# Kernel tuning notes

Hardware: AMD Instinct MI355X
Metric: run time of the kernel (lower is better)

The kernel has to match this reference:

```python
import jax, jax.numpy as jnp
import numpy as np

B, C, HD, H, W = 4, 64, 64, 64, 64  # batch, input_dim, hidden_dim, spatial


def conv1x1(x, w, b):
    # x: [B, Cin, H, W], w: [Cout, Cin], b: [Cout]
    return jnp.einsum('oc,bchw->bohw', w, x) + b[None, :, None, None]


def setup_inputs() -> dict:
    key = jax.random.key(0)
    ks = jax.random.split(key, 16)
    sc = lambda cin: 1.0 / np.sqrt(cin)
    d = {
        'h': jax.random.normal(ks[0], (B, C, H, W), jnp.float32),
        'm': jax.random.normal(ks[1], (B, C, H, W), jnp.float32),
        'Wq': jax.random.normal(ks[2], (HD, C), jnp.float32) * sc(C),
        'bq': jnp.zeros((HD,), jnp.float32),
        'Wk': jax.random.normal(ks[3], (HD, C), jnp.float32) * sc(C),
        'bk': jnp.zeros((HD,), jnp.float32),
        'Wk2': jax.random.normal(ks[4], (HD, C), jnp.float32) * sc(C),
        'bk2': jnp.zeros((HD,), jnp.float32),
        'Wv': jax.random.normal(ks[5], (C, C), jnp.float32) * sc(C),
        'bv': jnp.zeros((C,), jnp.float32),
        'Wv2': jax.random.normal(ks[6], (C, C), jnp.float32) * sc(C),
        'bv2': jnp.zeros((C,), jnp.float32),
        'Wz': jax.random.normal(ks[7], (2 * C, 2 * C), jnp.float32) * sc(2 * C),
        'bz': jnp.zeros((2 * C,), jnp.float32),
        'Wm': jax.random.normal(ks[8], (3 * C, 3 * C), jnp.float32) * sc(3 * C),
        'bm': jnp.zeros((3 * C,), jnp.float32),
    }
    return d


def reference(h, m, Wq, bq, Wk, bk, Wk2, bk2, Wv, bv, Wv2, bv2, Wz, bz, Wm, bm):
    b, c, hh, ww = h.shape
    n = hh * ww
    K_h = conv1x1(h, Wk, bk).reshape(b, HD, n)            # [B, HD, N]
    Q_h = conv1x1(h, Wq, bq).reshape(b, HD, n).transpose(0, 2, 1)  # [B, N, HD]
    V_h = conv1x1(h, Wv, bv).reshape(b, c, n)             # [B, C, N]
    K_m = conv1x1(m, Wk2, bk2).reshape(b, HD, n)
    V_m = conv1x1(m, Wv2, bv2).reshape(b, c, n)

    A_h = jax.nn.softmax(jnp.einsum('bnd,bdk->bnk', Q_h, K_h), axis=-1)  # [B, N, N]
    Z_h = jnp.einsum('bnk,bck->bcn', A_h, V_h).reshape(b, c, hh, ww)
    A_m = jax.nn.softmax(jnp.einsum('bnd,bdk->bnk', Q_h, K_m), axis=-1)
    Z_m = jnp.einsum('bnk,bck->bcn', A_m, V_m).reshape(b, c, hh, ww)

    Z = conv1x1(jnp.concatenate([Z_h, Z_m], axis=1), Wz, bz)   # [B, 2C, H, W]
    combined = conv1x1(jnp.concatenate([Z, h], axis=1), Wm, bm)  # [B, 3C, H, W]
    mo, mg, mi = jnp.split(combined, 3, axis=1)
    mi = jax.nn.sigmoid(mi)
    new_m = (1.0 - mi) * m + mi * jnp.tanh(mg)
    new_h = jax.nn.sigmoid(mo) * new_m
    return (new_h, new_m)
```

## Files before the change

kernel.cpp:

```cpp
#include <hip/hip_runtime.h>

#define BN 4
#define NN 4096
#define SPLITK 4
#define KTILE 64
#define LOG2E 1.44269504f
#define MFIX 36.0f

typedef __attribute__((ext_vector_type(8))) __bf16 bf16x8;
typedef __attribute__((ext_vector_type(8))) short s16x8;
typedef __attribute__((ext_vector_type(4))) float f32x4;
typedef unsigned short u16;

__device__ __forceinline__ u16 f2bf(float x) {
  unsigned int u = __builtin_bit_cast(unsigned int, x);
  u = (u + 0x7fffu + ((u >> 16) & 1u)) >> 16;
  return (u16)u;
}
__device__ __forceinline__ u16 f2bfs(float x) {
  __bf16 b = (__bf16)x;
  return __builtin_bit_cast(u16, b);
}
__device__ __forceinline__ float bf2f(u16 s) {
  unsigned int u = ((unsigned int)s) << 16;
  return __builtin_bit_cast(float, u);
}

__device__ __forceinline__ float fexp2(float x) {
#if defined(__HIP_DEVICE_COMPILE__) && __has_builtin(__builtin_amdgcn_exp2f)
  return __builtin_amdgcn_exp2f(x);
#else
  return __builtin_exp2f(x);
#endif
}

__device__ __forceinline__ f32x4 mfma32(bf16x8 a, bf16x8 b, f32x4 c) {
#if defined(__HIP_DEVICE_COMPILE__)
  return __builtin_amdgcn_mfma_f32_16x16x32_bf16(a, b, c, 0, 0, 0);
#else
  (void)a; (void)b;
  return c;
#endif
}

__device__ __forceinline__ void gld16(const u16* g, u16* l) {
#if defined(__HIP_DEVICE_COMPILE__)
  __builtin_amdgcn_global_load_lds(
      (const __attribute__((address_space(1))) void*)g,
      (__attribute__((address_space(3))) void*)l, 16, 0, 0);
#else
  (void)g; (void)l;
#endif
}

#if defined(__HIP_DEVICE_COMPILE__)
#define SETPRIO(p) __builtin_amdgcn_s_setprio(p)
#else
#define SETPRIO(p)
#endif

__global__ __launch_bounds__(256) void fuse_w2_kernel(
    const float* __restrict__ Wz, const float* __restrict__ bz,
    const float* __restrict__ Wm, const float* __restrict__ bm,
    const float* __restrict__ Wq, const float* __restrict__ Wk,
    const float* __restrict__ Wk2, const float* __restrict__ Wv,
    const float* __restrict__ Wv2,
    u16* __restrict__ Wbig, float* __restrict__ bbig, u16* __restrict__ Wall) {
  __shared__ float wrow[128];
  __shared__ float bzs[128];
  int t = threadIdx.x;
  if (blockIdx.x >= 192) {
    int pid = blockIdx.x - 192;
    const float* Wsrc = pid == 0 ? Wq : pid == 1 ? Wk : pid == 2 ? Wk2 : pid == 3 ? Wv : Wv2;
    float sc = (pid == 0) ? LOG2E : 1.f;
#pragma unroll
    for (int i = 0; i < 16; ++i) {
      int idx = t * 16 + i;
      float w = Wsrc[idx] * sc;
      u16 hu = f2bf(w);
      Wall[pid * 4096 + idx] = hu;
      Wall[5 * 4096 + pid * 4096 + idx] = f2bf(w - bf2f(hu));
    }
    return;
  }
  int o = blockIdx.x;
  if (t < 128) { wrow[t] = Wm[o * 192 + t]; bzs[t] = bz[t]; }
  __syncthreads();
  if (t < 128) {
    float s = 0.f;
#pragma unroll 4
    for (int j = 0; j < 128; ++j) s = fmaf(wrow[j], Wz[j * 128 + t], s);
    Wbig[o * 192 + t] = f2bf(s);
  } else if (t < 192) {
    Wbig[o * 192 + t] = f2bf(Wm[o * 192 + t]);
  } else if (t == 192) {
    float s = bm[o];
    for (int j = 0; j < 128; ++j) s = fmaf(wrow[j], bzs[j], s);
    bbig[o] = s;
  }
}

__global__ __launch_bounds__(256) void proj7_kernel(
    const u16* __restrict__ Wall,
    const float* __restrict__ bq, const float* __restrict__ bk,
    const float* __restrict__ bk2, const float* __restrict__ bv,
    const float* __restrict__ bv2,
    const float* __restrict__ h, const float* __restrict__ m,
    u16* __restrict__ Q, u16* __restrict__ Kh, u16* __restrict__ Km,
    u16* __restrict__ Vh, u16* __restrict__ Vm, u16* __restrict__ hT) {
  __shared__ float xs[64][65];
  int blk = blockIdx.x;
  int nt = blk & 63, b = (blk >> 6) & 3, src_m = blk >> 8;
  const float* src = src_m ? m : h;
  int t = threadIdx.x, lane = t & 63, w = t >> 6, col = lane & 15, quad = lane >> 4;
  int n0 = nt * 64;
  {
    int c0 = w * 16, nl = lane;
#pragma unroll
    for (int i = 0; i < 16; ++i)
      xs[c0 + i][nl] = src[((size_t)(b * 64) + c0 + i) * NN + n0 + nl];
  }
  __syncthreads();
  int nloc = w * 16 + col;
  bf16x8 xh[2], xl[2];
#pragma unroll
  for (int half = 0; half < 2; ++half) {
    bf16x8 hh, ll;
#pragma unroll
    for (int j = 0; j < 8; ++j) {
      float x = xs[half * 32 + quad * 8 + j][nloc];
      u16 hu = f2bf(x);
      hh[j] = __builtin_bit_cast(__bf16, hu);
      ll[j] = (__bf16)(x - bf2f(hu));
    }
    xh[half] = hh; xl[half] = ll;
  }
  if (!src_m) {
    int cj = lane & 7, nr = lane >> 3;
#pragma unroll
    for (int it = 0; it < 2; ++it) {
      int n = w * 16 + it * 8 + nr;
      bf16x8 hi8;
#pragma unroll
      for (int i = 0; i < 8; ++i)
        hi8[i] = __builtin_bit_cast(__bf16, f2bf(xs[cj * 8 + i][n]));
      *(bf16x8*)(void*)(hT + ((size_t)b * NN + n0 + n) * 64 + cj * 8) = hi8;
    }
  }
  int glob_n = n0 + nloc;
  auto do_proj = [&](int pid, const float* bias, u16* dstQK, u16* dstV) {
    const u16* Whi = Wall + pid * 4096;
    const u16* Wlo = Wall + 5 * 4096 + pid * 4096;
    float sc = (pid == 0) ? LOG2E : 1.f;
#pragma unroll
    for (int ot = 0; ot < 4; ++ot) {
      size_t wb = (size_t)(ot * 16 + col) * 64 + quad * 8;
      bf16x8 wh0 = *(const bf16x8*)(const void*)(Whi + wb);
      bf16x8 wh1 = *(const bf16x8*)(const void*)(Whi + wb + 32);
      bf16x8 wl0 = *(const bf16x8*)(const void*)(Wlo + wb);
      bf16x8 wl1 = *(const bf16x8*)(const void*)(Wlo + wb + 32);
      float4 b4 = *(const float4*)(bias + ot * 16 + quad * 4);
      f32x4 c = {b4.x * sc, b4.y * sc, b4.z * sc, b4.w * sc};
      c = mfma32(wh0, xh[0], c);
      c = mfma32(wh1, xh[1], c);
      c = mfma32(wh0, xl[0], c);
      c = mfma32(wh1, xl[1], c);
      c = mfma32(wl0, xh[0], c);
      c = mfma32(wl1, xh[1], c);
      if (dstQK) {
        uint2 p;
        p.x = (unsigned)f2bf(c[0]) | ((unsigned)f2bf(c[1]) << 16);
        p.y = (unsigned)f2bf(c[2]) | ((unsigned)f2bf(c[3]) << 16);
        *(uint2*)(void*)(dstQK + ((size_t)b * NN + glob_n) * 64 + ot * 16 + quad * 4) = p;
      } else {
        size_t base = ((size_t)b << 18) + (size_t)(glob_n >> 5) * 2048 + ot * 512 +
                      (size_t)((glob_n >> 3) & 3) * 128 + (glob_n & 7);
#pragma unroll
        for (int r = 0; r < 4; ++r) dstV[base + (quad * 4 + r) * 8] = f2bf(c[r]);
      }
    }
  };
  if (!src_m) {
    do_proj(0, bq, Q, nullptr);
    do_proj(1, bk, Kh, nullptr);
    do_proj(3, bv, nullptr, Vh);
  } else {
    do_proj(2, bk2, Km, nullptr);
    do_proj(4, bv2, nullptr, Vm);
  }
}

__global__ __launch_bounds__(256, 4) void flash11_kernel(
    const u16* __restrict__ Qg, const u16* __restrict__ Khg,
    const u16* __restrict__ Kmg, const u16* __restrict__ Vhg,
    const u16* __restrict__ Vmg, u16* __restrict__ Opart,
    float* __restrict__ Lpart) {
  __shared__ u16 Kl[2][4096];
  __shared__ u16 Vl[2][4096];
  int blk = blockIdx.x;
  int combo = blk & 31, qt = blk >> 5;
  int attn = combo & 1, b = (combo >> 1) & 3, split = combo >> 3;
  const u16* K = (attn ? Kmg : Khg) + (size_t)b * NN * 64;
  const u16* V = (attn ? Vmg : Vhg) + ((size_t)b << 18);
  int t = threadIdx.x, wave = t >> 6, lane = t & 63, col = lane & 15, quad = lane >> 4;
  int row0 = qt * 128 + wave * 32;

  bf16x8 bq[2][2];
#pragma unroll
  for (int g = 0; g < 2; ++g) {
    const u16* qp = Qg + (size_t)b * NN * 64 + (size_t)(row0 + g * 16 + col) * 64 + quad * 8;
    bq[g][0] = *(const bf16x8*)(const void*)qp;
    bq[g][1] = *(const bf16x8*)(const void*)(qp + 32);
  }

  f32x4 O[2][4];
#pragma unroll
  for (int g = 0; g < 2; ++g)
#pragma unroll
    for (int i = 0; i < 4; ++i) O[g][i] = f32x4{0.f, 0.f, 0.f, 0.f};
  f32x4 Lacc[2];
  Lacc[0] = f32x4{0.f, 0.f, 0.f, 0.f};
  Lacc[1] = f32x4{0.f, 0.f, 0.f, 0.f};
  const f32x4 minit = {-MFIX, -MFIX, -MFIX, -MFIX};
  s16x8 onesv;
#pragma unroll
  for (int i = 0; i < 8; ++i) onesv[i] = (short)0x3F80;
  bf16x8 ones8 = __builtin_bit_cast(bf16x8, onesv);
  int sp = split * 8 + b * 2 + attn;

  const int kbase = split * (NN / SPLITK);
  const int TILES = NN / SPLITK / KTILE;

#define STAGE(BUF, K0)                                                           \
  _Pragma("unroll") for (int jj = 0; jj < 2; ++jj) {                             \
    int p = jj * 256 + t;                                                        \
    int krow_ = p >> 3;                                                          \
    int kj_ = (p & 7) ^ (krow_ & 7);                                             \
    int s5_ = krow_ & 31;                                                        \
    int tr_ = (krow_ & 32) | ((s5_ & 12) << 1) | (((s5_ >> 4) & 1) << 2) | (s5_ & 3); \
    gld16(K + (size_t)((K0) + tr_) * 64 + kj_ * 8, &Kl[BUF][p * 8]);             \
    gld16(V + (size_t)(K0) * 64 + p * 8, &Vl[BUF][p * 8]);                       \
  }

  STAGE(0, kbase);

  for (int kt = 0; kt < TILES; ++kt) {
    __syncthreads();
    int cur = kt & 1;
    if (kt + 1 < TILES) { STAGE(cur ^ 1, kbase + (kt + 1) * KTILE); }
    const u16* Kb = &Kl[cur][0];
    const u16* Vb = &Vl[cur][0];
    f32x4 St[4][2];
    SETPRIO(1);
#pragma unroll
    for (int nt = 0; nt < 4; ++nt) {
      int row = nt * 16 + col;
      int ph0 = row * 8 + (quad ^ (col & 7));
      int ph1 = row * 8 + ((4 + quad) ^ (col & 7));
      bf16x8 a0 = *(const bf16x8*)(const void*)(Kb + ph0 * 8);
      bf16x8 a1 = *(const bf16x8*)(const void*)(Kb + ph1 * 8);
#pragma unroll
      for (int g = 0; g < 2; ++g) {
        f32x4 acc = mfma32(a0, bq[g][0], minit);
        acc = mfma32(a1, bq[g][1], acc);
        St[nt][g] = acc;
      }
    }
    SETPRIO(0);
    bf16x8 pa[2][2];
#pragma unroll
    for (int grp = 0; grp < 2; ++grp)
#pragma unroll
      for (int g = 0; g < 2; ++g) {
        s16x8 pf;
#pragma unroll
        for (int r = 0; r < 4; ++r) {
          pf[r] = (short)f2bfs(fexp2(St[2 * grp][g][r]));
          pf[r + 4] = (short)f2bfs(fexp2(St[2 * grp + 1][g][r]));
        }
        bf16x8 p8 = __builtin_bit_cast(bf16x8, pf);
        pa[grp][g] = p8;
        Lacc[g] = mfma32(p8, ones8, Lacc[g]);
      }
    const u16* vbase = Vb + lane * 8;
    SETPRIO(1);
#pragma unroll
    for (int grp = 0; grp < 2; ++grp)
#pragma unroll
      for (int ct = 0; ct < 4; ++ct) {
        bf16x8 vf = *(const bf16x8*)(const void*)(vbase + grp * 2048 + ct * 512);
        O[0][ct] = mfma32(pa[grp][0], vf, O[0][ct]);
        O[1][ct] = mfma32(pa[grp][1], vf, O[1][ct]);
      }
    SETPRIO(0);
  }
#undef STAGE

#pragma unroll
  for (int g = 0; g < 2; ++g) {
#pragma unroll
    for (int ct = 0; ct < 4; ++ct)
#pragma unroll
      for (int r = 0; r < 4; ++r) {
        size_t q = (size_t)row0 + g * 16 + quad * 4 + r;
        Opart[((size_t)sp * NN + q) * 64 + ct * 16 + col] = f2bfs(O[g][ct][r]);
      }
    if (col == 0) {
#pragma unroll
      for (int r = 0; r < 4; ++r)
        Lpart[(size_t)sp * NN + row0 + g * 16 + quad * 4 + r] = Lacc[g][r];
    }
  }
}

__global__ __launch_bounds__(256) void epi3_kernel(
    const u16* __restrict__ Wb, const float* __restrict__ bb,
    const u16* __restrict__ Opart, const float* __restrict__ Lpart,
    const u16* __restrict__ hT, const float* __restrict__ mglob,
    float* __restrict__ out) {
  int blk = blockIdx.x;
  int ng = blk * 16;
  int b = ng >> 12;
  int t = threadIdx.x, wave = t >> 6, lane = t & 63, col = lane & 15, quad = lane >> 4;
  int qb = (ng & (NN - 1)) + col;
  float Lh = 0.f, Lm = 0.f;
#pragma unroll
  for (int s = 0; s < SPLITK; ++s) {
    Lh += Lpart[(size_t)(s * 8 + b * 2) * NN + qb];
    Lm += Lpart[(size_t)(s * 8 + b * 2 + 1) * NN + qb];
  }
  float invLh = 1.f / Lh;
  float invLm = 1.f / Lm;
  size_t nrow = ((size_t)ng + col) * 64;
  bf16x8 bfr[6];
#define MERGEF(DST, ATTN, OFF, INVL)                                             \
  {                                                                              \
    float s8_[8] = {0.f, 0.f, 0.f, 0.f, 0.f, 0.f, 0.f, 0.f};                     \
    _Pragma("unroll") for (int sp_ = 0; sp_ < SPLITK; ++sp_) {                   \
      const u16* p_ =                                                            \
          Opart + ((size_t)(sp_ * 8 + b * 2 + (ATTN)) * NN + qb) * 64 + (OFF);   \
      bf16x8 a_ = *(const bf16x8*)(const void*)p_;                               \
      _Pragma("unroll") for (int i = 0; i < 8; ++i) s8_[i] += (float)a_[i];      \
    }                                                                            \
    bf16x8 r_;                                                                   \
    _Pragma("unroll") for (int i = 0; i < 8; ++i)                                \
      r_[i] = (__bf16)(s8_[i] * (INVL));                                         \
    DST = r_;                                                                    \
  }
  MERGEF(bfr[0], 0, quad * 8, invLh);
  MERGEF(bfr[1], 0, 32 + quad * 8, invLh);
  MERGEF(bfr[2], 1, quad * 8, invLm);
  MERGEF(bfr[3], 1, 32 + quad * 8, invLm);
#undef MERGEF
  bfr[4] = *(const bf16x8*)(const void*)(hT + nrow + quad * 8);
  bfr[5] = *(const bf16x8*)(const void*)(hT + nrow + 32 + quad * 8);
  f32x4 acc[3];
#pragma unroll
  for (int j = 0; j < 3; ++j) {
    int mt = wave + j * 4;
#pragma unroll
    for (int r = 0; r < 4; ++r) acc[j][r] = bb[mt * 16 + quad * 4 + r];
  }
#pragma unroll
  for (int ks = 0; ks < 6; ++ks) {
#pragma unroll
    for (int j = 0; j < 3; ++j) {
      int mt = wave + j * 4;
      bf16x8 af = *(const bf16x8*)(const void*)(Wb + (size_t)(mt * 16 + col) * 192 + ks * 32 + quad * 8);
      acc[j] = mfma32(af, bfr[ks], acc[j]);
    }
  }
  int nloc = (ng & (NN - 1)) + col;
#pragma unroll
  for (int r = 0; r < 4; ++r) {
    int o = wave * 16 + quad * 4 + r;
    float mo = acc[0][r], mgt = acc[1][r], mi = acc[2][r];
    float si = 1.f / (1.f + fexp2(-mi * LOG2E));
    float tg = 1.f - 2.f / (fexp2(2.f * LOG2E * mgt) + 1.f);
    float mv = mglob[(size_t)(b * 64 + o) * NN + nloc];
    float nm = (1.f - si) * mv + si * tg;
    float nh = nm / (1.f + fexp2(-mo * LOG2E));
    out[(size_t)(b * 64 + o) * NN + nloc] = nh;
    out[(size_t)BN * 64 * NN + (size_t)(b * 64 + o) * NN + nloc] = nm;
  }
}

extern "C" void kernel_launch(void* const* d_in, const int* in_sizes, int n_in,
                              void* d_out, int out_size, void* d_ws, size_t ws_size,
                              hipStream_t stream) {
  const float* h = (const float*)d_in[0];
  const float* m = (const float*)d_in[1];
  const float* Wq = (const float*)d_in[2];
  const float* bq = (const float*)d_in[3];
  const float* Wk = (const float*)d_in[4];
  const float* bk = (const float*)d_in[5];
  const float* Wk2 = (const float*)d_in[6];
  const float* bk2 = (const float*)d_in[7];
  const float* Wv = (const float*)d_in[8];
  const float* bv = (const float*)d_in[9];
  const float* Wv2 = (const float*)d_in[10];
  const float* bv2 = (const float*)d_in[11];
  const float* Wz = (const float*)d_in[12];
  const float* bz = (const float*)d_in[13];
  const float* Wm = (const float*)d_in[14];
  const float* bm = (const float*)d_in[15];
  float* out = (float*)d_out;

  size_t off = 0;
  auto alloc = [&](size_t bytes) {
    void* p = (char*)d_ws + off;
    off += (bytes + 255) & ~(size_t)255;
    return p;
  };
  const size_t bn64 = (size_t)BN * NN * 64;
  u16* Q  = (u16*)alloc(bn64 * 2);
  u16* Kh = (u16*)alloc(bn64 * 2);
  u16* Km = (u16*)alloc(bn64 * 2);
  u16* Vh = (u16*)alloc(bn64 * 2);
  u16* Vm = (u16*)alloc(bn64 * 2);
  u16* hT = (u16*)alloc(bn64 * 2);
  u16* Opart = (u16*)alloc((size_t)SPLITK * 8 * NN * 64 * 2);
  float* Lpart = (float*)alloc((size_t)SPLITK * 8 * NN * 4);
  u16* Wbigbf = (u16*)alloc(192 * 192 * 2);
  float* bbig = (float*)alloc(192 * 4);
  u16* Wall = (u16*)alloc((size_t)2 * 5 * 4096 * 2);
  (void)ws_size; (void)in_sizes; (void)n_in; (void)out_size;

  fuse_w2_kernel<<<197, 256, 0, stream>>>(Wz, bz, Wm, bm, Wq, Wk, Wk2, Wv, Wv2,
                                          Wbigbf, bbig, Wall);
  proj7_kernel<<<2 * BN * 64, 256, 0, stream>>>(Wall, bq, bk, bk2, bv, bv2, h, m,
                                                Q, Kh, Km, Vh, Vm, hT);
  flash11_kernel<<<32 * 32, 256, 0, stream>>>(Q, Kh, Km, Vh, Vm, Opart, Lpart);
  epi3_kernel<<<(BN * NN) / 16, 256, 0, stream>>>(Wbigbf, bbig, Opart, Lpart, hT, m, out);
}
```

Measured before the change: 167.7 us.

## Use 2 waves per block with 64 query rows per wave in flash kernel

The flash attention kernel now launches 128 threads per block, and each of the 2 waves handles 64 query rows instead of 32, so each K/V fragment read from LDS feeds twice as many MFMAs. K fragments are loaded once per tile and reused across two query-group passes, and global-to-LDS staging is spread over fewer threads. This cuts LDS read traffic per FLOP but raises register pressure (O and bq double) and halves the waves per block, which may lower occupancy and latency hiding.

```diff
diff --git a/kernel.cpp b/kernel.cpp
--- a/kernel.cpp
+++ b/kernel.cpp
@@ -190,7 +190,7 @@
   }
 }
 
-__global__ __launch_bounds__(256, 4) void flash11_kernel(
+__global__ __launch_bounds__(128, 2) void flash12_kernel(
     const u16* __restrict__ Qg, const u16* __restrict__ Khg,
     const u16* __restrict__ Kmg, const u16* __restrict__ Vhg,
     const u16* __restrict__ Vmg, u16* __restrict__ Opart,
@@ -203,24 +203,24 @@
   const u16* K = (attn ? Kmg : Khg) + (size_t)b * NN * 64;
   const u16* V = (attn ? Vmg : Vhg) + ((size_t)b << 18);
   int t = threadIdx.x, wave = t >> 6, lane = t & 63, col = lane & 15, quad = lane >> 4;
-  int row0 = qt * 128 + wave * 32;
-
-  bf16x8 bq[2][2];
-#pragma unroll
-  for (int g = 0; g < 2; ++g) {
+  int row0 = qt * 128 + wave * 64;
+
+  bf16x8 bq[4][2];
+#pragma unroll
+  for (int g = 0; g < 4; ++g) {
     const u16* qp = Qg + (size_t)b * NN * 64 + (size_t)(row0 + g * 16 + col) * 64 + quad * 8;
     bq[g][0] = *(const bf16x8*)(const void*)qp;
     bq[g][1] = *(const bf16x8*)(const void*)(qp + 32);
   }
 
-  f32x4 O[2][4];
-#pragma unroll
-  for (int g = 0; g < 2; ++g)
+  f32x4 O[4][4];
+#pragma unroll
+  for (int g = 0; g < 4; ++g)
 #pragma unroll
     for (int i = 0; i < 4; ++i) O[g][i] = f32x4{0.f, 0.f, 0.f, 0.f};
-  f32x4 Lacc[2];
-  Lacc[0] = f32x4{0.f, 0.f, 0.f, 0.f};
-  Lacc[1] = f32x4{0.f, 0.f, 0.f, 0.f};
+  f32x4 Lacc[4];
+#pragma unroll
+  for (int g = 0; g < 4; ++g) Lacc[g] = f32x4{0.f, 0.f, 0.f, 0.f};
   const f32x4 minit = {-MFIX, -MFIX, -MFIX, -MFIX};
   s16x8 onesv;
 #pragma unroll
@@ -232,8 +232,8 @@
   const int TILES = NN / SPLITK / KTILE;
 
 #define STAGE(BUF, K0)                                                           \
-  _Pragma("unroll") for (int jj = 0; jj < 2; ++jj) {                             \
-    int p = jj * 256 + t;                                                        \
+  _Pragma("unroll") for (int jj = 0; jj < 4; ++jj) {                             \
+    int p = jj * 128 + t;                                                        \
     int krow_ = p >> 3;                                                          \
     int kj_ = (p & 7) ^ (krow_ & 7);                                             \
     int s5_ = krow_ & 31;                                                        \
@@ -250,38 +250,43 @@
     if (kt + 1 < TILES) { STAGE(cur ^ 1, kbase + (kt + 1) * KTILE); }
     const u16* Kb = &Kl[cur][0];
     const u16* Vb = &Vl[cur][0];
-    f32x4 St[4][2];
-    SETPRIO(1);
+    bf16x8 a0[4], a1[4];
 #pragma unroll
     for (int nt = 0; nt < 4; ++nt) {
       int row = nt * 16 + col;
-      int ph0 = row * 8 + (quad ^ (col & 7));
-      int ph1 = row * 8 + ((4 + quad) ^ (col & 7));
-      bf16x8 a0 = *(const bf16x8*)(const void*)(Kb + ph0 * 8);
-      bf16x8 a1 = *(const bf16x8*)(const void*)(Kb + ph1 * 8);
-#pragma unroll
-      for (int g = 0; g < 2; ++g) {
-        f32x4 acc = mfma32(a0, bq[g][0], minit);
-        acc = mfma32(a1, bq[g][1], acc);
-        St[nt][g] = acc;
-      }
-    }
-    SETPRIO(0);
-    bf16x8 pa[2][2];
-#pragma unroll
-    for (int grp = 0; grp < 2; ++grp)
-#pragma unroll
-      for (int g = 0; g < 2; ++g) {
-        s16x8 pf;
-#pragma unroll
-        for (int r = 0; r < 4; ++r) {
-          pf[r] = (short)f2bfs(fexp2(St[2 * grp][g][r]));
-          pf[r + 4] = (short)f2bfs(fexp2(St[2 * grp + 1][g][r]));
+      a0[nt] = *(const bf16x8*)(const void*)(Kb + (row * 8 + (quad ^ (col & 7))) * 8);
+      a1[nt] = *(const bf16x8*)(const void*)(Kb + (row * 8 + ((4 + quad) ^ (col & 7))) * 8);
+    }
+    bf16x8 pa[2][4];
+#pragma unroll
+    for (int gp = 0; gp < 2; ++gp) {
+      f32x4 St[4][2];
+      SETPRIO(1);
+#pragma unroll
+      for (int nt = 0; nt < 4; ++nt)
+#pragma unroll
+        for (int gg = 0; gg < 2; ++gg) {
+          int g = gp * 2 + gg;
+          f32x4 acc = mfma32(a0[nt], bq[g][0], minit);
+          acc = mfma32(a1[nt], bq[g][1], acc);
+          St[nt][gg] = acc;
         }
-        bf16x8 p8 = __builtin_bit_cast(bf16x8, pf);
-        pa[grp][g] = p8;
-        Lacc[g] = mfma32(p8, ones8, Lacc[g]);
-      }
+      SETPRIO(0);
+#pragma unroll
+      for (int grp = 0; grp < 2; ++grp)
+#pragma unroll
+        for (int gg = 0; gg < 2; ++gg) {
+          s16x8 pf;
+#pragma unroll
+          for (int r = 0; r < 4; ++r) {
+            pf[r] = (short)f2bfs(fexp2(St[2 * grp][gg][r]));
+            pf[r + 4] = (short)f2bfs(fexp2(St[2 * grp + 1][gg][r]));
+          }
+          bf16x8 p8 = __builtin_bit_cast(bf16x8, pf);
+          pa[grp][gp * 2 + gg] = p8;
+          Lacc[gp * 2 + gg] = mfma32(p8, ones8, Lacc[gp * 2 + gg]);
+        }
+    }
     const u16* vbase = Vb + lane * 8;
     SETPRIO(1);
 #pragma unroll
@@ -289,15 +294,15 @@
 #pragma unroll
       for (int ct = 0; ct < 4; ++ct) {
         bf16x8 vf = *(const bf16x8*)(const void*)(vbase + grp * 2048 + ct * 512);
-        O[0][ct] = mfma32(pa[grp][0], vf, O[0][ct]);
-        O[1][ct] = mfma32(pa[grp][1], vf, O[1][ct]);
+#pragma unroll
+        for (int g = 0; g < 4; ++g) O[g][ct] = mfma32(pa[grp][g], vf, O[g][ct]);
       }
     SETPRIO(0);
   }
 #undef STAGE
 
 #pragma unroll
-  for (int g = 0; g < 2; ++g) {
+  for (int g = 0; g < 4; ++g) {
 #pragma unroll
     for (int ct = 0; ct < 4; ++ct)
 #pragma unroll
@@ -430,6 +435,6 @@
                                           Wbigbf, bbig, Wall);
   proj7_kernel<<<2 * BN * 64, 256, 0, stream>>>(Wall, bq, bk, bk2, bv, bv2, h, m,
                                                 Q, Kh, Km, Vh, Vm, hT);
-  flash11_kernel<<<32 * 32, 256, 0, stream>>>(Q, Kh, Km, Vh, Vm, Opart, Lpart);
+  flash12_kernel<<<32 * 32, 128, 0, stream>>>(Q, Kh, Km, Vh, Vm, Opart, Lpart);
   epi3_kernel<<<(BN * NN) / 16, 256, 0, stream>>>(Wbigbf, bbig, Opart, Lpart, hT, m, out);
 }
```

After: 169.7 us. No clear change (+1.2%).

## Software-pipeline PV matmul one tile behind QK with triple-buffered V

Applied to the files above, without the earlier changes.

Restructures the flash attention loop so that each iteration's P·V MFMAs use the probabilities from the previous tile, placed between the QK^T MFMAs and the exp/bf16 conversion of the current tile. The goal is to let the exp and convert work overlap with matrix-core work instead of serialising QK, softmax and PV. V gets a third shared-memory buffer so the previous tile's V is still resident while the next tile is being staged. Shared memory per block rises from 32 KB to 40 KB, which could reduce occupancy, and more registers stay live across iterations.

```diff
diff --git a/kernel.cpp b/kernel.cpp
--- a/kernel.cpp
+++ b/kernel.cpp
@@ -190,13 +190,13 @@
   }
 }
 
-__global__ __launch_bounds__(256, 4) void flash11_kernel(
+__global__ __launch_bounds__(256, 4) void flash13_kernel(
     const u16* __restrict__ Qg, const u16* __restrict__ Khg,
     const u16* __restrict__ Kmg, const u16* __restrict__ Vhg,
     const u16* __restrict__ Vmg, u16* __restrict__ Opart,
     float* __restrict__ Lpart) {
   __shared__ u16 Kl[2][4096];
-  __shared__ u16 Vl[2][4096];
+  __shared__ u16 Vl[3][4096];
   int blk = blockIdx.x;
   int combo = blk & 31, qt = blk >> 5;
   int attn = combo & 1, b = (combo >> 1) & 3, split = combo >> 3;
@@ -221,6 +221,11 @@
   f32x4 Lacc[2];
   Lacc[0] = f32x4{0.f, 0.f, 0.f, 0.f};
   Lacc[1] = f32x4{0.f, 0.f, 0.f, 0.f};
+  bf16x8 pa[2][2];
+#pragma unroll
+  for (int grp = 0; grp < 2; ++grp)
+#pragma unroll
+    for (int g = 0; g < 2; ++g) pa[grp][g] = bf16x8{};
   const f32x4 minit = {-MFIX, -MFIX, -MFIX, -MFIX};
   s16x8 onesv;
 #pragma unroll
@@ -231,25 +236,29 @@
   const int kbase = split * (NN / SPLITK);
   const int TILES = NN / SPLITK / KTILE;
 
-#define STAGE(BUF, K0)                                                           \
+#define STAGE(KB, VB, K0)                                                        \
   _Pragma("unroll") for (int jj = 0; jj < 2; ++jj) {                             \
     int p = jj * 256 + t;                                                        \
     int krow_ = p >> 3;                                                          \
     int kj_ = (p & 7) ^ (krow_ & 7);                                             \
     int s5_ = krow_ & 31;                                                        \
     int tr_ = (krow_ & 32) | ((s5_ & 12) << 1) | (((s5_ >> 4) & 1) << 2) | (s5_ & 3); \
-    gld16(K + (size_t)((K0) + tr_) * 64 + kj_ * 8, &Kl[BUF][p * 8]);             \
-    gld16(V + (size_t)(K0) * 64 + p * 8, &Vl[BUF][p * 8]);                       \
-  }
-
-  STAGE(0, kbase);
+    gld16(K + (size_t)((K0) + tr_) * 64 + kj_ * 8, (KB) + p * 8);                \
+    gld16(V + (size_t)(K0) * 64 + p * 8, (VB) + p * 8);                          \
+  }
+
+  STAGE(&Kl[0][0], &Vl[0][0], kbase);
+  int vs_cur = 0;
 
   for (int kt = 0; kt < TILES; ++kt) {
+    int cur = kt & 1;
+    int vs_nxt = (vs_cur == 2) ? 0 : vs_cur + 1;
+    int vs_prv = (vs_cur == 0) ? 2 : vs_cur - 1;
     __syncthreads();
-    int cur = kt & 1;
-    if (kt + 1 < TILES) { STAGE(cur ^ 1, kbase + (kt + 1) * KTILE); }
+    if (kt + 1 < TILES) {
+      STAGE(&Kl[cur ^ 1][0], &Vl[vs_nxt][0], kbase + (kt + 1) * KTILE);
+    }
     const u16* Kb = &Kl[cur][0];
-    const u16* Vb = &Vl[cur][0];
     f32x4 St[4][2];
     SETPRIO(1);
 #pragma unroll
@@ -267,7 +276,19 @@
       }
     }
     SETPRIO(0);
-    bf16x8 pa[2][2];
+    if (kt > 0) {
+      const u16* vbase = &Vl[vs_prv][0] + lane * 8;
+      SETPRIO(1);
+#pragma unroll
+      for (int grp = 0; grp < 2; ++grp)
+#pragma unroll
+        for (int ct = 0; ct < 4; ++ct) {
+          bf16x8 vf = *(const bf16x8*)(const void*)(vbase + grp * 2048 + ct * 512);
+          O[0][ct] = mfma32(pa[grp][0], vf, O[0][ct]);
+          O[1][ct] = mfma32(pa[grp][1], vf, O[1][ct]);
+        }
+      SETPRIO(0);
+    }
 #pragma unroll
     for (int grp = 0; grp < 2; ++grp)
 #pragma unroll
@@ -282,8 +303,12 @@
         pa[grp][g] = p8;
         Lacc[g] = mfma32(p8, ones8, Lacc[g]);
       }
-    const u16* vbase = Vb + lane * 8;
-    SETPRIO(1);
+    vs_cur = vs_nxt;
+  }
+#undef STAGE
+  {
+    int vs_prv = (vs_cur == 0) ? 2 : vs_cur - 1;
+    const u16* vbase = &Vl[vs_prv][0] + lane * 8;
 #pragma unroll
     for (int grp = 0; grp < 2; ++grp)
 #pragma unroll
@@ -292,9 +317,7 @@
         O[0][ct] = mfma32(pa[grp][0], vf, O[0][ct]);
         O[1][ct] = mfma32(pa[grp][1], vf, O[1][ct]);
       }
-    SETPRIO(0);
-  }
-#undef STAGE
+  }
 
 #pragma unroll
   for (int g = 0; g < 2; ++g) {
@@ -430,6 +453,6 @@
                                           Wbigbf, bbig, Wall);
   proj7_kernel<<<2 * BN * 64, 256, 0, stream>>>(Wall, bq, bk, bk2, bv, bv2, h, m,
                                                 Q, Kh, Km, Vh, Vm, hT);
-  flash11_kernel<<<32 * 32, 256, 0, stream>>>(Q, Kh, Km, Vh, Vm, Opart, Lpart);
+  flash13_kernel<<<32 * 32, 256, 0, stream>>>(Q, Kh, Km, Vh, Vm, Opart, Lpart);
   epi3_kernel<<<(BN * NN) / 16, 256, 0, stream>>>(Wbigbf, bbig, Opart, Lpart, hT, m, out);
 }
```

Result: no change. 170.3 us (+1.5%).
